# Kernel optimization log

Measured on AMD Instinct MI355X. Metric: run time of the kernel, lower is better.

The kernel has to match this reference:

```python
import jax, jax.numpy as jnp
import numpy as np

NEG_SLOPE = 0.2  # PyG GATConv default negative_slope
NUM_GRAPHS = 64


def gat_conv(x, src, dst, W, a_src, a_dst, bias, concat):
    """PyG-style GATConv (eval mode, self-loops already appended to src/dst)."""
    N = x.shape[0]
    H, C = a_src.shape
    h = (x @ W).reshape(N, H, C)                      # [N,H,C]
    al_s = jnp.sum(h * a_src, axis=-1)                # [N,H]
    al_d = jnp.sum(h * a_dst, axis=-1)                # [N,H]
    e = jax.nn.leaky_relu(al_s[src] + al_d[dst], NEG_SLOPE)  # [E,H]
    # numerically-stable segment softmax over incoming edges of each dst node
    m = jax.ops.segment_max(e, dst, num_segments=N)   # [N,H]
    ex = jnp.exp(e - m[dst])
    denom = jax.ops.segment_sum(ex, dst, num_segments=N)
    alpha = ex / (denom[dst] + 1e-16)                 # [E,H]
    out = jax.ops.segment_sum(h[src] * alpha[:, :, None], dst, num_segments=N)  # [N,H,C]
    out = out.reshape(N, H * C) if concat else out.mean(axis=1)
    return out + bias


def setup_inputs() -> dict:
    key = jax.random.key(0)
    ks = jax.random.split(key, 32)
    N, E, F_in, H = 20000, 100000, 128, 8
    x = jax.random.normal(ks[0], (N, F_in), jnp.float32)
    edge_index = jax.random.randint(ks[1], (2, E), 0, N, dtype=jnp.int32)
    batch = jnp.sort(jax.random.randint(ks[2], (N,), 0, NUM_GRAPHS, dtype=jnp.int32))
    inp = {"x": x, "edge_index": edge_index, "batch": batch}
    # (fan_in, per-head channels) for conv1..conv_final
    dims = [(F_in, 64), (512, 256), (2048, 256), (2048, 256), (2048, 256)]
    ki = 3
    for i, (fi, c) in enumerate(dims, 1):
        concat = i < 5
        inp[f"W{i}"] = jax.random.normal(ks[ki], (fi, H * c), jnp.float32) * (1.0 / np.sqrt(fi)); ki += 1
        inp[f"a_src{i}"] = jax.random.normal(ks[ki], (H, c), jnp.float32) * 0.1; ki += 1
        inp[f"a_dst{i}"] = jax.random.normal(ks[ki], (H, c), jnp.float32) * 0.1; ki += 1
        inp[f"b{i}"] = jnp.zeros((H * c if concat else c,), jnp.float32)
    inp["W_lin"] = jax.random.normal(ks[ki], (256, 128), jnp.float32) * (1.0 / np.sqrt(256))
    inp["b_lin"] = jnp.zeros((128,), jnp.float32)
    return inp


def reference(x, edge_index, batch,
              W1, a_src1, a_dst1, b1,
              W2, a_src2, a_dst2, b2,
              W3, a_src3, a_dst3, b3,
              W4, a_src4, a_dst4, b4,
              W5, a_src5, a_dst5, b5,
              W_lin, b_lin):
    N = x.shape[0]
    loop = jnp.arange(N, dtype=edge_index.dtype)  # GATConv add_self_loops=True
    src = jnp.concatenate([edge_index[0], loop])
    dst = jnp.concatenate([edge_index[1], loop])
    h = jax.nn.elu(gat_conv(x, src, dst, W1, a_src1, a_dst1, b1, True))
    h = jax.nn.elu(gat_conv(h, src, dst, W2, a_src2, a_dst2, b2, True))
    h = jax.nn.elu(gat_conv(h, src, dst, W3, a_src3, a_dst3, b3, True))
    h = jax.nn.elu(gat_conv(h, src, dst, W4, a_src4, a_dst4, b4, True))
    h = jax.nn.elu(gat_conv(h, src, dst, W5, a_src5, a_dst5, b5, False))
    sums = jax.ops.segment_sum(h, batch, num_segments=NUM_GRAPHS)
    counts = jax.ops.segment_sum(jnp.ones((N, 1), h.dtype), batch, num_segments=NUM_GRAPHS)
    pooled = jax.nn.elu(sums / jnp.maximum(counts, 1.0))  # global_mean_pool + elu
    return pooled @ W_lin + b_lin
```

## Files before the change

kernel.cpp:

```cpp
#include <hip/hip_runtime.h>
#include <hip/hip_fp16.h>
#include <math.h>

#define NHEADS 8
#define NG 64

typedef _Float16 half8_t __attribute__((ext_vector_type(8)));
typedef _Float16 half4_t __attribute__((ext_vector_type(4)));
typedef float    float4_t __attribute__((ext_vector_type(4)));
typedef __attribute__((address_space(1))) const void g_void;
typedef __attribute__((address_space(3))) void l_void;

__device__ __forceinline__ float elu_f(float x)   { return x > 0.f ? x : expf(x) - 1.f; }
__device__ __forceinline__ float lrelu_f(float x) { return x >= 0.f ? x : 0.2f * x; }

__device__ __forceinline__ float4 ld4(const float* p) { return *(const float4*)p; }
__device__ __forceinline__ float4 ld4(const __half* p) {
    const __half2* q = (const __half2*)p;
    __half2 a = q[0], b = q[1];
    return make_float4(__half2float(a.x), __half2float(a.y),
                       __half2float(b.x), __half2float(b.y));
}
__device__ __forceinline__ void st4(float* p, float4 v) { *(float4*)p = v; }
__device__ __forceinline__ void st4(__half* p, float4 v) {
    __half2 a, b;
    a.x = __float2half(v.x); a.y = __float2half(v.y);
    b.x = __float2half(v.z); b.y = __float2half(v.w);
    __half2* q = (__half2*)p; q[0] = a; q[1] = b;
}
__device__ __forceinline__ float scl(float v)  { return v; }
__device__ __forceinline__ float scl(__half v) { return __half2float(v); }
__device__ __forceinline__ void sst(float* p, float v)  { *p = v; }
__device__ __forceinline__ void sst(__half* p, float v) { *p = __float2half(v); }

struct h4s { __half a, b, c, d; };

__global__ void hist_kernel(const int* __restrict__ ei, int E, int Etot, int* __restrict__ counts) {
    int e = blockIdx.x * blockDim.x + threadIdx.x;
    if (e >= Etot) return;
    int dst = (e < E) ? ei[E + e] : (e - E);
    atomicAdd(&counts[dst], 1);
}

__global__ __launch_bounds__(256) void scan_kernel(const int* __restrict__ counts,
                                                   int* __restrict__ offsets,
                                                   int* __restrict__ cursor, int N) {
    __shared__ int wsum[4];
    const int tid = threadIdx.x;
    const int lane = tid & 63, wid = tid >> 6;
    int carry = 0;
    for (int base = 0; base < N; base += 1024) {
        int i0 = base + tid * 4;
        int v0 = 0, v1 = 0, v2 = 0, v3 = 0;
        if (i0 + 3 < N) {
            int4 q = *(const int4*)(counts + i0);
            v0 = q.x; v1 = q.y; v2 = q.z; v3 = q.w;
        } else {
            if (i0     < N) v0 = counts[i0];
            if (i0 + 1 < N) v1 = counts[i0 + 1];
            if (i0 + 2 < N) v2 = counts[i0 + 2];
            if (i0 + 3 < N) v3 = counts[i0 + 3];
        }
        int tsum = v0 + v1 + v2 + v3;
        int incl = tsum;
#pragma unroll
        for (int off = 1; off < 64; off <<= 1) {
            int t = __shfl_up(incl, off);
            if (lane >= off) incl += t;
        }
        if (lane == 63) wsum[wid] = incl;
        __syncthreads();
        int woff = carry;
        for (int w = 0; w < wid; ++w) woff += wsum[w];
        int o0 = woff + incl - tsum;
        int o1 = o0 + v0, o2 = o1 + v1, o3 = o2 + v2;
        if (i0     < N) { offsets[i0]     = o0; cursor[i0]     = o0; }
        if (i0 + 1 < N) { offsets[i0 + 1] = o1; cursor[i0 + 1] = o1; }
        if (i0 + 2 < N) { offsets[i0 + 2] = o2; cursor[i0 + 2] = o2; }
        if (i0 + 3 < N) { offsets[i0 + 3] = o3; cursor[i0 + 3] = o3; }
        __syncthreads();
        carry += wsum[0] + wsum[1] + wsum[2] + wsum[3];
    }
    if (tid == 0) offsets[N] = carry;
}

__global__ void scatter_kernel(const int* __restrict__ ei, int E, int Etot,
                               int* __restrict__ cursor, int* __restrict__ perm_src) {
    int e = blockIdx.x * blockDim.x + threadIdx.x;
    if (e >= Etot) return;
    int src, dst;
    if (e < E) { src = ei[e]; dst = ei[E + e]; }
    else       { src = e - E; dst = e - E; }
    int pos = atomicAdd(&cursor[dst], 1);
    perm_src[pos] = src;
}

struct PrepArgs {
    const float* x; __half* x16; long n4;
    const float* W[5]; __half* T[5];
    int K[5], Nn[5];
    int b0;
    int tb[5];
};

__global__ __launch_bounds__(256) void prep_kernel(PrepArgs a) {
    int bid = blockIdx.x;
    if (bid < a.b0) {
        long i = (long)bid * 256 + threadIdx.x;
        if (i < a.n4) {
            float4 v = ((const float4*)a.x)[i];
            h4s o; o.a = __float2half(v.x); o.b = __float2half(v.y);
            o.c = __float2half(v.z); o.d = __float2half(v.w);
            ((h4s*)a.x16)[i] = o;
        }
        return;
    }
    int l = 0, base = a.b0;
#pragma unroll
    for (int j = 0; j < 4; ++j) if (bid >= a.tb[j]) { l = j + 1; base = a.tb[j]; }
    const float* W = a.W[l]; __half* T = a.T[l];
    int K = a.K[l], Nn = a.Nn[l];
    int t = bid - base;
    int tilesx = Nn >> 5;
    int nb = (t % tilesx) * 32, kb = (t / tilesx) * 32;
    __shared__ float tt[32][33];
    int tx = threadIdx.x & 31, ty = threadIdx.x >> 5;
#pragma unroll
    for (int r = 0; r < 32; r += 8)
        tt[ty + r][tx] = W[(size_t)(kb + ty + r) * Nn + nb + tx];
    __syncthreads();
#pragma unroll
    for (int r = 0; r < 32; r += 8)
        T[(size_t)(nb + ty + r) * K + kb + tx] = __float2half(tt[tx][ty + r]);
}

#define MMA_PHASE(MH, NH)                                                      \
  __builtin_amdgcn_s_setprio(1);                                               \
  { _Pragma("unroll") for (int f_ = 0; f_ < 4; ++f_) {                         \
      _Pragma("unroll") for (int g_ = 0; g_ < 2; ++g_) {                       \
        _Pragma("unroll") for (int kk_ = 0; kk_ < 2; ++kk_)                    \
          acc[(MH) * 2 + (NH)][f_][g_] =                                       \
              __builtin_amdgcn_mfma_f32_16x16x32_f16(                          \
                  af[f_][kk_], bf[g_][kk_],                                    \
                  acc[(MH) * 2 + (NH)][f_][g_], 0, 0, 0);                      \
  } } }                                                                        \
  __builtin_amdgcn_s_setprio(0);

template <bool FUSE_AL>
__global__ __launch_bounds__(512, 2) void gemm_mfma256_kernel(const __half* __restrict__ A,
                                                              const __half* __restrict__ Bt,
                                                              __half* __restrict__ C,
                                                              const float* __restrict__ a_src,
                                                              const float* __restrict__ a_dst,
                                                              float* __restrict__ al_s,
                                                              float* __restrict__ al_d,
                                                              int M, int N, int K) {
    __shared__ __half lds[2][2][16384];
    const int tid  = threadIdx.x;
    const int lane = tid & 63;
    const int wave = tid >> 6;
    const int wr   = wave >> 2;
    const int wc   = wave & 3;

    const int nwg = (int)(gridDim.x * gridDim.y);
    const int lin = (int)(blockIdx.y * gridDim.x + blockIdx.x);
    const int q = nwg >> 3, r = nwg & 7;
    const int xcd = lin & 7, idx = lin >> 3;
    const int nid = (xcd < r ? xcd * (q + 1) : r * (q + 1) + (xcd - r) * q) + idx;
    const int bx = nid % (int)gridDim.x;
    const int by = nid / (int)gridDim.x;
    const int row0 = by * 256;
    const int col0 = bx * 256;

    const int l15 = lane & 15, l4 = lane >> 4;
    const int srow = tid >> 3;
    const int kch  = (tid & 7) ^ (srow & 7);

    float4_t acc[4][4][2];
#pragma unroll
    for (int i = 0; i < 4; ++i)
#pragma unroll
        for (int j = 0; j < 4; ++j)
#pragma unroll
            for (int g = 0; g < 2; ++g)
                acc[i][j][g] = (float4_t){0.f, 0.f, 0.f, 0.f};

    auto stageA = [&](int cb, int kt, int halfsel) {
#pragma unroll
        for (int sub = 0; sub < 2; ++sub) {
            int rr = halfsel * 128 + sub * 64 + srow;
            int gr = row0 + rr; if (gr >= M) gr = M - 1;
            const __half* g = A + (size_t)gr * K + kt * 64 + kch * 8;
            __half* l = &lds[cb][0][(halfsel * 128 + sub * 64) * 64] + tid * 8;
            __builtin_amdgcn_global_load_lds((g_void*)g, (l_void*)l, 16, 0, 0);
        }
    };
    auto stageB = [&](int cb, int kt, int halfsel) {
#pragma unroll
        for (int sub = 0; sub < 2; ++sub) {
            int rr = halfsel * 128 + sub * 64 + srow;
            const __half* g = Bt + (size_t)(col0 + rr) * K + kt * 64 + kch * 8;
            __half* l = &lds[cb][1][(halfsel * 128 + sub * 64) * 64] + tid * 8;
            __builtin_amdgcn_global_load_lds((g_void*)g, (l_void*)l, 16, 0, 0);
        }
    };

    half8_t af[4][2], bf[2][2];
    auto ldA = [&](int cb, int mh) {
        const char* base = (const char*)&lds[cb][0][0];
#pragma unroll
        for (int f = 0; f < 4; ++f) {
            int row = mh * 128 + wr * 64 + f * 16 + l15;
#pragma unroll
            for (int kk = 0; kk < 2; ++kk) {
                int ch = (kk * 4 + l4) ^ (row & 7);
                af[f][kk] = *(const half8_t*)(base + row * 128 + ch * 16);
            }
        }
    };
    auto ldB = [&](int cb, int nh) {
        const char* base = (const char*)&lds[cb][1][0];
#pragma unroll
        for (int f = 0; f < 2; ++f) {
            int row = nh * 128 + wc * 32 + f * 16 + l15;
#pragma unroll
            for (int kk = 0; kk < 2; ++kk) {
                int ch = (kk * 4 + l4) ^ (row & 7);
                bf[f][kk] = *(const half8_t*)(base + row * 128 + ch * 16);
            }
        }
    };

    const int nt = K >> 6;
    stageA(0, 0, 0); stageB(0, 0, 0); stageB(0, 0, 1); stageA(0, 0, 1);

    for (int t = 0; t < nt; ++t) {
        int cb = t & 1, nb = cb ^ 1;
        int ktn = (t + 1 < nt) ? t + 1 : t;

        stageA(nb, ktn, 0);
        __builtin_amdgcn_sched_barrier(0);
        asm volatile("s_waitcnt vmcnt(6)" ::: "memory");
        __builtin_amdgcn_s_barrier();
        __builtin_amdgcn_sched_barrier(0);
        ldA(cb, 0); ldB(cb, 0);
        MMA_PHASE(0, 0)

        stageB(nb, ktn, 0);
        __builtin_amdgcn_sched_barrier(0);
        asm volatile("s_waitcnt vmcnt(6)" ::: "memory");
        __builtin_amdgcn_s_barrier();
        __builtin_amdgcn_sched_barrier(0);
        ldB(cb, 1);
        MMA_PHASE(0, 1)

        stageB(nb, ktn, 1);
        __builtin_amdgcn_sched_barrier(0);
        asm volatile("s_waitcnt vmcnt(6)" ::: "memory");
        __builtin_amdgcn_s_barrier();
        __builtin_amdgcn_sched_barrier(0);
        ldA(cb, 1);
        MMA_PHASE(1, 1)

        stageA(nb, ktn, 1);
        ldB(cb, 0);
        MMA_PHASE(1, 0)
    }

#pragma unroll
    for (int mh = 0; mh < 2; ++mh) {
#pragma unroll
        for (int nh = 0; nh < 2; ++nh) {
#pragma unroll
            for (int fm = 0; fm < 4; ++fm) {
#pragma unroll
                for (int r2 = 0; r2 < 4; ++r2) {
                    int row = row0 + mh * 128 + wr * 64 + fm * 16 + l4 * 4 + r2;
                    if (row < M) {
#pragma unroll
                        for (int fn = 0; fn < 2; ++fn) {
                            int col = col0 + nh * 128 + wc * 32 + fn * 16 + l15;
                            C[(size_t)row * N + col] = __float2half(acc[mh * 2 + nh][fm][fn][r2]);
                        }
                    }
                }
            }
        }
    }

    if constexpr (FUSE_AL) {
        const int h = bx;
        float as_v[2][2], ad_v[2][2];
#pragma unroll
        for (int nh = 0; nh < 2; ++nh)
#pragma unroll
            for (int fn = 0; fn < 2; ++fn) {
                int cc = nh * 128 + wc * 32 + fn * 16 + l15;
                as_v[nh][fn] = a_src[h * 256 + cc];
                ad_v[nh][fn] = a_dst[h * 256 + cc];
            }
        asm volatile("s_waitcnt vmcnt(0)" ::: "memory");
        __syncthreads();
        float* al_lds = (float*)&lds[0][0][0];
#pragma unroll
        for (int mh = 0; mh < 2; ++mh)
#pragma unroll
            for (int fm = 0; fm < 4; ++fm)
#pragma unroll
                for (int r2 = 0; r2 < 4; ++r2) {
                    float ps = 0.f, pd = 0.f;
#pragma unroll
                    for (int nh = 0; nh < 2; ++nh)
#pragma unroll
                        for (int fn = 0; fn < 2; ++fn) {
                            float v = acc[mh * 2 + nh][fm][fn][r2];
                            ps += v * as_v[nh][fn];
                            pd += v * ad_v[nh][fn];
                        }
#pragma unroll
                    for (int o = 1; o < 16; o <<= 1) {
                        ps += __shfl_xor(ps, o);
                        pd += __shfl_xor(pd, o);
                    }
                    if (l15 == 0) {
                        int rrow = mh * 128 + wr * 64 + fm * 16 + l4 * 4 + r2;
                        al_lds[(rrow * 4 + wc) * 2 + 0] = ps;
                        al_lds[(rrow * 4 + wc) * 2 + 1] = pd;
                    }
                }
        __syncthreads();
        if (tid < 256) {
            int grow = row0 + tid;
            if (grow < M) {
                float s = al_lds[(tid * 4 + 0) * 2] + al_lds[(tid * 4 + 1) * 2] +
                          al_lds[(tid * 4 + 2) * 2] + al_lds[(tid * 4 + 3) * 2];
                float d = al_lds[(tid * 4 + 0) * 2 + 1] + al_lds[(tid * 4 + 1) * 2 + 1] +
                          al_lds[(tid * 4 + 2) * 2 + 1] + al_lds[(tid * 4 + 3) * 2 + 1];
                al_s[(size_t)grow * 8 + h] = s;
                al_d[(size_t)grow * 8 + h] = d;
            }
        }
    }
}

template <typename TA, typename TC>
__global__ __launch_bounds__(256) void gemm_kernel(const TA* __restrict__ A,
                                                   const float* __restrict__ B,
                                                   TC* __restrict__ C,
                                                   int M, int N, int K) {
    __shared__ float As[16][64];
    __shared__ float Bs[16][64];
    const int tid  = threadIdx.x;
    const int row0 = blockIdx.y * 64, col0 = blockIdx.x * 64;
    const int am = tid >> 2, ak = (tid & 3) << 2;
    const int bk = tid >> 4, bn = (tid & 15) << 2;
    const int ty = (tid >> 4) << 2, tx = (tid & 15) << 2;
    float acc[4][4] = {};
    const int arow = row0 + am;
    for (int k0 = 0; k0 < K; k0 += 16) {
        float4 a4 = make_float4(0.f, 0.f, 0.f, 0.f);
        if (arow < M) a4 = ld4(A + (size_t)arow * K + k0 + ak);
        As[ak + 0][am] = a4.x; As[ak + 1][am] = a4.y;
        As[ak + 2][am] = a4.z; As[ak + 3][am] = a4.w;
        *(float4*)&Bs[bk][bn] = *(const float4*)(B + (size_t)(k0 + bk) * N + col0 + bn);
        __syncthreads();
#pragma unroll
        for (int k = 0; k < 16; ++k) {
            float4 ar = *(const float4*)&As[k][ty];
            float4 br = *(const float4*)&Bs[k][tx];
            acc[0][0] += ar.x * br.x; acc[0][1] += ar.x * br.y; acc[0][2] += ar.x * br.z; acc[0][3] += ar.x * br.w;
            acc[1][0] += ar.y * br.x; acc[1][1] += ar.y * br.y; acc[1][2] += ar.y * br.z; acc[1][3] += ar.y * br.w;
            acc[2][0] += ar.z * br.x; acc[2][1] += ar.z * br.y; acc[2][2] += ar.z * br.z; acc[2][3] += ar.z * br.w;
            acc[3][0] += ar.w * br.x; acc[3][1] += ar.w * br.y; acc[3][2] += ar.w * br.z; acc[3][3] += ar.w * br.w;
        }
        __syncthreads();
    }
#pragma unroll
    for (int i = 0; i < 4; ++i) {
        int r = row0 + ty + i;
        if (r < M) {
            float4 o = make_float4(acc[i][0], acc[i][1], acc[i][2], acc[i][3]);
            st4(C + (size_t)r * N + col0 + tx, o);
        }
    }
}

__global__ void al_vec64_kernel(const __half* __restrict__ ht, const float* __restrict__ a_src,
                                const float* __restrict__ a_dst, float* __restrict__ al_s,
                                float* __restrict__ al_d, int N) {
    long wid  = (long)((blockIdx.x * blockDim.x + threadIdx.x) >> 6);
    int lane = threadIdx.x & 63;
    int sub = lane >> 4, l16 = lane & 15;
    long pair = wid * 4 + sub;
    if (pair >= (long)N * NHEADS) return;
    int n = (int)(pair >> 3), h = (int)(pair & 7);
    const __half* hp = ht + (size_t)n * 512 + h * 64 + l16 * 4;
    half4_t v = *(const half4_t*)hp;
    float4 as4 = *(const float4*)(a_src + h * 64 + l16 * 4);
    float4 ad4 = *(const float4*)(a_dst + h * 64 + l16 * 4);
    float v0 = (float)v[0], v1 = (float)v[1], v2 = (float)v[2], v3 = (float)v[3];
    float ss = v0 * as4.x + v1 * as4.y + v2 * as4.z + v3 * as4.w;
    float sd = v0 * ad4.x + v1 * ad4.y + v2 * ad4.z + v3 * ad4.w;
#pragma unroll
    for (int off = 8; off > 0; off >>= 1) {
        ss += __shfl_down(ss, off);
        sd += __shfl_down(sd, off);
    }
    if (l16 == 0) { al_s[pair] = ss; al_d[pair] = sd; }
}

template <int HC, int C, int MODE>
__global__ __launch_bounds__(256) void agg_fused_kernel(const __half* __restrict__ ht,
                                                        const float* __restrict__ al_s,
                                                        const float* __restrict__ al_d,
                                                        const int* __restrict__ offsets,
                                                        const int* __restrict__ perm_src,
                                                        const float* __restrict__ bias,
                                                        void* __restrict__ outv, int N) {
    constexpr int V = HC / 256;
    int n = blockIdx.x;
    int tid = threadIdx.x;
    int lane = tid & 63;
    const int head = (tid * V) / C;
    int s = offsets[n], e = offsets[n + 1];

    int h2 = lane & 7, es = lane >> 3;
    float ad2 = al_d[(size_t)n * 8 + h2];
    float m = -1e30f;
    for (int p0 = s + es; p0 < e; p0 += 8)
        m = fmaxf(m, lrelu_f(al_s[(size_t)perm_src[p0] * 8 + h2] + ad2));
#pragma unroll
    for (int off = 8; off < 64; off <<= 1) m = fmaxf(m, __shfl_xor(m, off));
    float den = 0.f;
    for (int p0 = s + es; p0 < e; p0 += 8)
        den += expf(lrelu_f(al_s[(size_t)perm_src[p0] * 8 + h2] + ad2) - m);
#pragma unroll
    for (int off = 8; off < 64; off <<= 1) den += __shfl_xor(den, off);
    float inv0 = 1.f / (den + 1e-16f);
    float mh   = __shfl(m, head);
    float invh = __shfl(inv0, head);
    float adh  = __shfl(ad2, head);

    float acc[V];
#pragma unroll
    for (int i = 0; i < V; ++i) acc[i] = 0.f;
    const __half* base = ht + (size_t)tid * V;
    int p = s;
    for (; p + 4 <= e; p += 4) {
        int s0 = perm_src[p], s1 = perm_src[p + 1], s2 = perm_src[p + 2], s3 = perm_src[p + 3];
        float a0 = expf(lrelu_f(al_s[(size_t)s0 * 8 + head] + adh) - mh);
        float a1 = expf(lrelu_f(al_s[(size_t)s1 * 8 + head] + adh) - mh);
        float a2 = expf(lrelu_f(al_s[(size_t)s2 * 8 + head] + adh) - mh);
        float a3 = expf(lrelu_f(al_s[(size_t)s3 * 8 + head] + adh) - mh);
        if (V == 8) {
            half8_t v0 = *(const half8_t*)(base + (size_t)s0 * HC);
            half8_t v1 = *(const half8_t*)(base + (size_t)s1 * HC);
            half8_t v2 = *(const half8_t*)(base + (size_t)s2 * HC);
            half8_t v3 = *(const half8_t*)(base + (size_t)s3 * HC);
#pragma unroll
            for (int i = 0; i < 8; ++i) acc[i] += a0 * (float)v0[i];
#pragma unroll
            for (int i = 0; i < 8; ++i) acc[i] += a1 * (float)v1[i];
#pragma unroll
            for (int i = 0; i < 8; ++i) acc[i] += a2 * (float)v2[i];
#pragma unroll
            for (int i = 0; i < 8; ++i) acc[i] += a3 * (float)v3[i];
        } else {
            __half2 w0 = *(const __half2*)(base + (size_t)s0 * HC);
            __half2 w1 = *(const __half2*)(base + (size_t)s1 * HC);
            __half2 w2 = *(const __half2*)(base + (size_t)s2 * HC);
            __half2 w3 = *(const __half2*)(base + (size_t)s3 * HC);
            acc[0] += a0 * __half2float(w0.x); acc[1] += a0 * __half2float(w0.y);
            acc[0] += a1 * __half2float(w1.x); acc[1] += a1 * __half2float(w1.y);
            acc[0] += a2 * __half2float(w2.x); acc[1] += a2 * __half2float(w2.y);
            acc[0] += a3 * __half2float(w3.x); acc[1] += a3 * __half2float(w3.y);
        }
    }
    for (; p < e; ++p) {
        int src = perm_src[p];
        float a = expf(lrelu_f(al_s[(size_t)src * 8 + head] + adh) - mh);
        const __half* hp = base + (size_t)src * HC;
        if (V == 8) {
            half8_t v = *(const half8_t*)hp;
#pragma unroll
            for (int i = 0; i < 8; ++i) acc[i] += a * (float)v[i];
        } else {
            __half2 v2 = *(const __half2*)hp;
            acc[0] += a * __half2float(v2.x);
            acc[1] += a * __half2float(v2.y);
        }
    }
    if (MODE == 0) {
        __half* out = (__half*)outv;
        if (V == 8) {
            half8_t o;
#pragma unroll
            for (int i = 0; i < 8; ++i)
                o[i] = (_Float16)elu_f(acc[i] * invh + bias[tid * 8 + i]);
            *(half8_t*)(out + (size_t)n * HC + tid * 8) = o;
        } else {
            __half2 o;
            o.x = __float2half(elu_f(acc[0] * invh + bias[tid * 2 + 0]));
            o.y = __float2half(elu_f(acc[1] * invh + bias[tid * 2 + 1]));
            *(__half2*)(out + (size_t)n * HC + tid * 2) = o;
        }
    } else {
        __shared__ float sm[256][8];
#pragma unroll
        for (int i = 0; i < 8; ++i) sm[tid][i] = acc[i] * invh;
        __syncthreads();
        float ssum = 0.f;
#pragma unroll
        for (int h = 0; h < 8; ++h) ssum += sm[h * 32 + (tid >> 3)][tid & 7];
        float* out = (float*)outv;
        out[(size_t)n * C + tid] = elu_f(ssum * (1.f / NHEADS) + bias[tid]);
    }
}

template <typename TH>
__global__ void al_kernel(const TH* __restrict__ ht, const float* __restrict__ a_src,
                          const float* __restrict__ a_dst, float* __restrict__ al_s,
                          float* __restrict__ al_d, int N, int C) {
    int wid  = (int)((blockIdx.x * blockDim.x + threadIdx.x) >> 6);
    int lane = threadIdx.x & 63;
    if (wid >= N * NHEADS) return;
    int n = wid / NHEADS, h = wid % NHEADS;
    const TH* hp = ht + (size_t)n * (NHEADS * C) + h * C;
    float ss = 0.f, sd = 0.f;
    for (int c = lane; c < C; c += 64) {
        float v = scl(hp[c]);
        ss += v * a_src[h * C + c];
        sd += v * a_dst[h * C + c];
    }
#pragma unroll
    for (int off = 32; off > 0; off >>= 1) {
        ss += __shfl_down(ss, off);
        sd += __shfl_down(sd, off);
    }
    if (lane == 0) { al_s[wid] = ss; al_d[wid] = sd; }
}

__global__ void alpha_kernel(const int* __restrict__ offsets, const int* __restrict__ perm_src,
                             const float* __restrict__ al_s, const float* __restrict__ al_d,
                             float* __restrict__ alpha, int N) {
    int idx = blockIdx.x * blockDim.x + threadIdx.x;
    if (idx >= N * NHEADS) return;
    int n = idx / NHEADS, h = idx % NHEADS;
    int s = offsets[n], e = offsets[n + 1];
    float ad = al_d[idx];
    float m = -1e30f;
    for (int p = s; p < e; ++p) {
        float v = lrelu_f(al_s[perm_src[p] * NHEADS + h] + ad);
        m = fmaxf(m, v);
    }
    float denom = 0.f;
    for (int p = s; p < e; ++p) {
        float v  = lrelu_f(al_s[perm_src[p] * NHEADS + h] + ad);
        float ex = expf(v - m);
        alpha[(size_t)p * NHEADS + h] = ex;
        denom += ex;
    }
    float inv = 1.f / (denom + 1e-16f);
    for (int p = s; p < e; ++p) alpha[(size_t)p * NHEADS + h] *= inv;
}

template <int HC, int C, int MODE, typename TH, typename TO>
__global__ __launch_bounds__(256) void agg_kernel(const TH* __restrict__ ht,
                                                  const float* __restrict__ alpha,
                                                  const int* __restrict__ offsets,
                                                  const int* __restrict__ perm_src,
                                                  const float* __restrict__ bias,
                                                  TO* __restrict__ out, int N) {
    constexpr int PER = HC / 256;
    int n = blockIdx.x;
    int tid = threadIdx.x;
    float acc[PER];
#pragma unroll
    for (int i = 0; i < PER; ++i) acc[i] = 0.f;
    int s = offsets[n], e = offsets[n + 1];
    for (int p = s; p < e; ++p) {
        int src = perm_src[p];
        const TH* hp = ht + (size_t)src * HC;
#pragma unroll
        for (int i = 0; i < PER; ++i) {
            int j = tid + i * 256;
            float a = alpha[(size_t)p * NHEADS + (j / C)];
            acc[i] += a * scl(hp[j]);
        }
    }
    if (MODE == 0) {
#pragma unroll
        for (int i = 0; i < PER; ++i) {
            int j = tid + i * 256;
            sst(&out[(size_t)n * HC + j], elu_f(acc[i] + bias[j]));
        }
    } else {
        float srow = 0.f;
#pragma unroll
        for (int i = 0; i < PER; ++i) srow += acc[i];
        sst(&out[(size_t)n * C + tid], elu_f(srow * (1.f / NHEADS) + bias[tid]));
    }
}

__global__ void gstart_kernel(const int* __restrict__ batch, int* __restrict__ gstart, int N) {
    int n = blockIdx.x * blockDim.x + threadIdx.x;
    if (n > N) return;
    if (n == 0) {
        int b0 = batch[0];
        for (int g = 0; g <= b0; ++g) gstart[g] = 0;
    } else if (n == N) {
        int bl = batch[N - 1];
        for (int g = bl + 1; g <= NG; ++g) gstart[g] = N;
    } else {
        int bp = batch[n - 1], bc = batch[n];
        for (int g = bp + 1; g <= bc; ++g) gstart[g] = n;
    }
}

__global__ void pool_kernel(const float* __restrict__ h5, const int* __restrict__ gstart,
                            float* __restrict__ pooled) {
    int g = blockIdx.x, c = threadIdx.x;
    int s = gstart[g], e = gstart[g + 1];
    float sum = 0.f;
    for (int n = s; n < e; ++n) sum += h5[(size_t)n * 256 + c];
    float cnt = fmaxf((float)(e - s), 1.f);
    pooled[g * 256 + c] = elu_f(sum / cnt);
}

__global__ void linear_kernel(const float* __restrict__ pooled, const float* __restrict__ W,
                              const float* __restrict__ b, float* __restrict__ out) {
    int g = blockIdx.x, c = threadIdx.x;
    float s = b[c];
    for (int k = 0; k < 256; ++k) s += pooled[g * 256 + k] * W[k * 128 + c];
    out[g * 128 + c] = s;
}

__device__ __forceinline__ int lb_dev(const int* a, int n, int key) {
    int lo = 0, hi = n;
    while (lo < hi) { int mid = (lo + hi) >> 1; if (a[mid] < key) lo = mid + 1; else hi = mid; }
    return lo;
}

__global__ __launch_bounds__(256) void pool_linear_kernel(const float* __restrict__ h5,
                                                          const int* __restrict__ batch, int N,
                                                          const float* __restrict__ Wlin,
                                                          const float* __restrict__ blin,
                                                          float* __restrict__ out) {
    int g = blockIdx.x, c = threadIdx.x;
    int s = lb_dev(batch, N, g);
    int e = lb_dev(batch, N, g + 1);
    __shared__ float pooled_s[256];
    float sum = 0.f;
    for (int n = s; n < e; ++n) sum += h5[(size_t)n * 256 + c];
    float cnt = fmaxf((float)(e - s), 1.f);
    pooled_s[c] = elu_f(sum / cnt);
    __syncthreads();
    if (c < 128) {
        float acc = blin[c];
        for (int k = 0; k < 256; ++k) acc += pooled_s[k] * Wlin[k * 128 + c];
        out[g * 128 + c] = acc;
    }
}

template <typename TIO, typename TH>
static void run_pipeline(const float* x, const float* const* W, const float* const* asrc,
                         const float* const* adst, const float* const* bias,
                         char* rawIO, char* rawHT,
                         float* al_s, float* al_d, float* alpha_buf,
                         const int* offsets, const int* perm_src,
                         int N, hipStream_t stream) {
    TIO* bufIO = (TIO*)rawIO;
    TH*  bufHT = (TH*)rawHT;
    {
        dim3 g(512 / 64, (N + 63) / 64);
        gemm_kernel<float, TH><<<g, 256, 0, stream>>>(x, W[0], bufHT, N, 512, 128);
        al_kernel<TH><<<(N * NHEADS * 64 + 255) / 256, 256, 0, stream>>>(bufHT, asrc[0], adst[0], al_s, al_d, N, 64);
        alpha_kernel<<<(N * NHEADS + 255) / 256, 256, 0, stream>>>(offsets, perm_src, al_s, al_d, alpha_buf, N);
        agg_kernel<512, 64, 0, TH, TIO><<<N, 256, 0, stream>>>(bufHT, alpha_buf, offsets, perm_src, bias[0], bufIO, N);
    }
    int Kdim = 512;
    for (int l = 1; l < 5; ++l) {
        dim3 g(2048 / 64, (N + 63) / 64);
        gemm_kernel<TIO, TH><<<g, 256, 0, stream>>>(bufIO, W[l], bufHT, N, 2048, Kdim);
        al_kernel<TH><<<(N * NHEADS * 64 + 255) / 256, 256, 0, stream>>>(bufHT, asrc[l], adst[l], al_s, al_d, N, 256);
        alpha_kernel<<<(N * NHEADS + 255) / 256, 256, 0, stream>>>(offsets, perm_src, al_s, al_d, alpha_buf, N);
        if (l < 4)
            agg_kernel<2048, 256, 0, TH, TIO><<<N, 256, 0, stream>>>(bufHT, alpha_buf, offsets, perm_src, bias[l], bufIO, N);
        else
            agg_kernel<2048, 256, 1, TH, float><<<N, 256, 0, stream>>>(bufHT, alpha_buf, offsets, perm_src, bias[l], (float*)rawIO, N);
        Kdim = 2048;
    }
}

extern "C" void kernel_launch(void* const* d_in, const int* in_sizes, int n_in,
                              void* d_out, int out_size, void* d_ws, size_t ws_size,
                              hipStream_t stream) {
    const float* x     = (const float*)d_in[0];
    const int*   ei    = (const int*)d_in[1];
    const int*   batch = (const int*)d_in[2];
    const float* W[5]    = {(const float*)d_in[3],  (const float*)d_in[7],  (const float*)d_in[11],
                            (const float*)d_in[15], (const float*)d_in[19]};
    const float* asrc[5] = {(const float*)d_in[4],  (const float*)d_in[8],  (const float*)d_in[12],
                            (const float*)d_in[16], (const float*)d_in[20]};
    const float* adst[5] = {(const float*)d_in[5],  (const float*)d_in[9],  (const float*)d_in[13],
                            (const float*)d_in[17], (const float*)d_in[21]};
    const float* bias[5] = {(const float*)d_in[6],  (const float*)d_in[10], (const float*)d_in[14],
                            (const float*)d_in[18], (const float*)d_in[22]};
    const float* Wlin = (const float*)d_in[23];
    const float* blin = (const float*)d_in[24];

    const int N    = in_sizes[0] / 128;
    const int E    = in_sizes[1] / 2;
    const int Etot = E + N;

    auto align256 = [](size_t b) { return (b + 255) & ~(size_t)255; };

    size_t sz_counts = align256((size_t)N * 4);
    size_t sz_off    = align256((size_t)(N + 1) * 4);
    size_t sz_cur    = align256((size_t)N * 4);
    size_t sz_perm   = align256((size_t)Etot * 4);
    size_t sz_al     = align256((size_t)N * NHEADS * 4);
    size_t sz_alpha  = align256((size_t)Etot * NHEADS * 4);
    size_t sz_gst    = align256((size_t)(NG + 1) * 4);
    size_t sz_pool   = align256((size_t)NG * 256 * 4);
    size_t misc = sz_counts + sz_off + sz_cur + sz_perm + 2 * sz_al + sz_alpha + sz_gst + sz_pool;

    size_t bigf  = align256((size_t)N * 2048 * sizeof(float));
    size_t bigh  = align256((size_t)N * 2048 * sizeof(__half));
    const int Kd[5] = {128, 512, 2048, 2048, 2048};
    const int Nd[5] = {512, 2048, 2048, 2048, 2048};
    size_t sz_wt_each[5], sz_wt_all = 0;
    for (int l = 0; l < 5; ++l) { sz_wt_each[l] = align256((size_t)Kd[l] * Nd[l] * sizeof(__half)); sz_wt_all += sz_wt_each[l]; }
    size_t sz_x16 = align256((size_t)N * 128 * sizeof(__half));

    int path;
    if      (ws_size >= misc + 2 * bigh + sz_wt_all + sz_x16) path = 3;
    else if (ws_size >= misc + 2 * bigf)                      path = 0;
    else if (ws_size >= misc + bigf + bigh)                   path = 1;
    else if (ws_size >= misc + 2 * bigh)                      path = 2;
    else {
        hipMemsetAsync(d_out, 0, (size_t)out_size * sizeof(float), stream);
        return;
    }

    char* ws = (char*)d_ws;
    size_t off = 0;
    auto carve = [&](size_t bytes) { void* p = ws + off; off += bytes; return p; };
    int*   counts   = (int*)carve(sz_counts);
    int*   offsets  = (int*)carve(sz_off);
    int*   cursor   = (int*)carve(sz_cur);
    int*   perm_src = (int*)carve(sz_perm);
    float* al_s     = (float*)carve(sz_al);
    float* al_d     = (float*)carve(sz_al);
    float* alpha    = (float*)carve(sz_alpha);
    int*   gstart   = (int*)carve(sz_gst);
    float* pooled   = (float*)carve(sz_pool);

    hipMemsetAsync(counts, 0, (size_t)N * 4, stream);
    hist_kernel<<<(Etot + 255) / 256, 256, 0, stream>>>(ei, E, Etot, counts);
    scan_kernel<<<1, 256, 0, stream>>>(counts, offsets, cursor, N);
    scatter_kernel<<<(Etot + 255) / 256, 256, 0, stream>>>(ei, E, Etot, cursor, perm_src);

    if (path == 3) {
        char*   rawIO = (char*)carve(bigh);
        char*   rawHT = (char*)carve(bigh);
        __half* Wt[5];
        for (int l = 0; l < 5; ++l) Wt[l] = (__half*)carve(sz_wt_each[l]);
        __half* x16   = (__half*)carve(sz_x16);
        __half* bufIO = (__half*)rawIO;
        __half* bufHT = (__half*)rawHT;

        PrepArgs pa;
        pa.x = x; pa.x16 = x16; pa.n4 = (long)N * 128 / 4;
        for (int l = 0; l < 5; ++l) { pa.W[l] = W[l]; pa.T[l] = Wt[l]; pa.K[l] = Kd[l]; pa.Nn[l] = Nd[l]; }
        int bacc = (int)((pa.n4 + 255) / 256);
        pa.b0 = bacc;
        for (int l = 0; l < 5; ++l) { bacc += (Nd[l] / 32) * (Kd[l] / 32); pa.tb[l] = bacc; }
        prep_kernel<<<bacc, 256, 0, stream>>>(pa);

        const __half* curA = x16;
        int Kdim = 128;
        for (int l = 0; l < 5; ++l) {
            const int C  = (l == 0) ? 64 : 256;
            const int HC = NHEADS * C;
            dim3 gg(HC / 256, (N + 255) / 256);
            if (l == 0) {
                gemm_mfma256_kernel<false><<<gg, 512, 0, stream>>>(curA, Wt[l], bufHT,
                                                                   nullptr, nullptr, nullptr, nullptr,
                                                                   N, HC, Kdim);
                al_vec64_kernel<<<(N * NHEADS * 16 + 255) / 256, 256, 0, stream>>>(bufHT, asrc[l], adst[l], al_s, al_d, N);
            } else {
                gemm_mfma256_kernel<true><<<gg, 512, 0, stream>>>(curA, Wt[l], bufHT,
                                                                  asrc[l], adst[l], al_s, al_d,
                                                                  N, HC, Kdim);
            }
            if (l == 0)
                agg_fused_kernel<512, 64, 0><<<N, 256, 0, stream>>>(bufHT, al_s, al_d, offsets, perm_src, bias[l], bufIO, N);
            else if (l < 4)
                agg_fused_kernel<2048, 256, 0><<<N, 256, 0, stream>>>(bufHT, al_s, al_d, offsets, perm_src, bias[l], bufIO, N);
            else
                agg_fused_kernel<2048, 256, 1><<<N, 256, 0, stream>>>(bufHT, al_s, al_d, offsets, perm_src, bias[l], (float*)rawIO, N);
            curA = bufIO;
            Kdim = (l == 0) ? 512 : 2048;
        }
        pool_linear_kernel<<<NG, 256, 0, stream>>>((const float*)rawIO, batch, N, Wlin, blin, (float*)d_out);
        return;
    }

    char* rawIO = (char*)carve(path == 2 ? bigh : bigf);
    char* rawHT = (char*)carve(path == 0 ? bigf : bigh);

    if (path == 0)
        run_pipeline<float, float>(x, W, asrc, adst, bias, rawIO, rawHT, al_s, al_d, alpha, offsets, perm_src, N, stream);
    else if (path == 1)
        run_pipeline<float, __half>(x, W, asrc, adst, bias, rawIO, rawHT, al_s, al_d, alpha, offsets, perm_src, N, stream);
    else
        run_pipeline<__half, __half>(x, W, asrc, adst, bias, rawIO, rawHT, al_s, al_d, alpha, offsets, perm_src, N, stream);

    gstart_kernel<<<(N + 1 + 255) / 256, 256, 0, stream>>>(batch, gstart, N);
    pool_kernel<<<NG, 256, 0, stream>>>((const float*)rawIO, gstart, pooled);
    linear_kernel<<<NG, 128, 0, stream>>>(pooled, Wlin, blin, (float*)d_out);
}
```

Measured before the change: 1.164 ms.

## Reorder GEMM main loop: issue LDS fragment reads before global staging, add barriers

Restructures the MFMA GEMM K-loop schedule so each phase reads its LDS fragments first, then issues the next tile's global-to-LDS stage, then waits (vmcnt 4) and barriers before the MFMA phase. It adds a barrier after every MMA phase and an initial wait and barrier after the prologue. The goal is to overlap LDS reads with global loads and tighten synchronisation in the double-buffered pipeline. The cost is more barriers per iteration, and a changed wait-count scheme that could stall or race if the counts don't match the number of loads in flight.

```diff
diff --git a/kernel.cpp b/kernel.cpp
--- a/kernel.cpp
+++ b/kernel.cpp
@@ -146,6 +146,9 @@
   } } }                                                                        \
   __builtin_amdgcn_s_setprio(0);
 
+#define SBAR  __builtin_amdgcn_s_barrier()
+#define SCHB  __builtin_amdgcn_sched_barrier(0)
+
 template <bool FUSE_AL>
 __global__ __launch_bounds__(512, 2) void gemm_mfma256_kernel(const __half* __restrict__ A,
                                                               const __half* __restrict__ Bt,
@@ -233,38 +236,53 @@
 
     const int nt = K >> 6;
     stageA(0, 0, 0); stageB(0, 0, 0); stageB(0, 0, 1); stageA(0, 0, 1);
+    SCHB;
+    asm volatile("s_waitcnt vmcnt(4)" ::: "memory");
+    SBAR;
+    SCHB;
 
     for (int t = 0; t < nt; ++t) {
         int cb = t & 1, nb = cb ^ 1;
         int ktn = (t + 1 < nt) ? t + 1 : t;
 
+        ldA(cb, 0); ldB(cb, 0);
         stageA(nb, ktn, 0);
-        __builtin_amdgcn_sched_barrier(0);
-        asm volatile("s_waitcnt vmcnt(6)" ::: "memory");
-        __builtin_amdgcn_s_barrier();
-        __builtin_amdgcn_sched_barrier(0);
-        ldA(cb, 0); ldB(cb, 0);
+        SCHB;
+        asm volatile("s_waitcnt vmcnt(4)" ::: "memory");
+        SBAR;
+        SCHB;
         MMA_PHASE(0, 0)
-
+        SBAR;
+        SCHB;
+
+        ldB(cb, 1);
         stageB(nb, ktn, 0);
-        __builtin_amdgcn_sched_barrier(0);
-        asm volatile("s_waitcnt vmcnt(6)" ::: "memory");
-        __builtin_amdgcn_s_barrier();
-        __builtin_amdgcn_sched_barrier(0);
-        ldB(cb, 1);
+        SCHB;
+        asm volatile("s_waitcnt vmcnt(4)" ::: "memory");
+        SBAR;
+        SCHB;
         MMA_PHASE(0, 1)
-
+        SBAR;
+        SCHB;
+
+        ldA(cb, 1);
         stageB(nb, ktn, 1);
-        __builtin_amdgcn_sched_barrier(0);
-        asm volatile("s_waitcnt vmcnt(6)" ::: "memory");
-        __builtin_amdgcn_s_barrier();
-        __builtin_amdgcn_sched_barrier(0);
-        ldA(cb, 1);
+        SCHB;
+        SBAR;
+        SCHB;
         MMA_PHASE(1, 1)
-
+        SBAR;
+        SCHB;
+
+        ldB(cb, 0);
         stageA(nb, ktn, 1);
-        ldB(cb, 0);
+        SCHB;
+        asm volatile("s_waitcnt vmcnt(4)" ::: "memory");
+        SBAR;
+        SCHB;
         MMA_PHASE(1, 0)
+        SBAR;
+        SCHB;
     }
 
 #pragma unroll
```

Result: no change. 1.169 ms (+0.4%).
